# Kernel optimization log

Measured on AMD Instinct MI355X. Metric: run time of the kernel, lower is better.

## Reference

```python
import jax, jax.numpy as jnp
import numpy as np

B, N, D, H = 1, 512, 128, 128  # batch, n_res, d_pair, d_hid
EPS = 1e-5


def _layer_norm(x, w, b):
    m = jnp.mean(x, axis=-1, keepdims=True)
    v = jnp.mean(jnp.square(x - m), axis=-1, keepdims=True)
    return (x - m) * jax.lax.rsqrt(v + EPS) * w + b


def setup_inputs() -> dict:
    key = jax.random.key(0)
    ks = jax.random.split(key, 8)
    s = 0.02
    return {
        "z": jax.random.normal(ks[0], (B, N, N, D), dtype=jnp.float32),
        "mask": jnp.ones((B, N, N), dtype=jnp.float32),
        "ln_in_w": jnp.ones((D,), dtype=jnp.float32),
        "ln_in_b": jnp.zeros((D,), dtype=jnp.float32),
        "w_ab_p": jax.random.normal(ks[1], (2 * H, D), dtype=jnp.float32) * s,
        "b_ab_p": jnp.zeros((2 * H,), dtype=jnp.float32),
        "w_ab_g": jax.random.normal(ks[2], (2 * H, D), dtype=jnp.float32) * s,
        "b_ab_g": jnp.zeros((2 * H,), dtype=jnp.float32),
        "w_g": jax.random.normal(ks[3], (D, D), dtype=jnp.float32) * s,
        "ln_out_w": jnp.ones((H,), dtype=jnp.float32),
        "ln_out_b": jnp.zeros((H,), dtype=jnp.float32),
        "w_z": jax.random.normal(ks[4], (D, H), dtype=jnp.float32) * s,
    }


def reference(z, mask, ln_in_w, ln_in_b, w_ab_p, b_ab_p, w_ab_g, b_ab_g, w_g, ln_out_w, ln_out_b, w_z):
    # mask: [B,N,N] -> [B,N,N,1], scaled by N**-0.5 (non-alphafold-original mode)
    m = mask[..., None] * (mask.shape[-1] ** -0.5)
    zl = _layer_norm(z, ln_in_w, ln_in_b)              # [B,N,N,D]
    g = jnp.einsum('bijd,ed->bije', zl, w_g)           # gate logits, no bias
    ab = (jnp.einsum('bijd,hd->bijh', zl, w_ab_p) + b_ab_p) \
         * m * jax.nn.sigmoid(jnp.einsum('bijd,hd->bijh', zl, w_ab_g) + b_ab_g)
    a, b = jnp.split(ab, 2, axis=-1)                   # each [B,N,N,H]
    # outgoing triangle update: x[b,i,j,h] = sum_k a[b,i,k,h] * b[b,j,k,h]
    x = jnp.einsum('bikh,bjkh->bijh', a, b)
    x = _layer_norm(x, ln_out_w, ln_out_b)
    x = jnp.einsum('bijh,dh->bijd', x, w_z)            # linear_z, no bias
    return x, g
```

## Files before the change

### kernel.cpp

```cpp
#include <hip/hip_runtime.h>
#include <hip/hip_bf16.h>

#define NRES 512
#define DDIM 128
#define HDIM 128
#define NPOS (NRES * NRES)
#define PLANE ((size_t)HDIM * NPOS)
#define EPSF 1e-5f
#define INV_SQRT_N 0.044194173824159216f

typedef __attribute__((ext_vector_type(4))) float  floatx4;
typedef __attribute__((ext_vector_type(8))) short  shortx8;

__device__ __forceinline__ short f2bf(float f) {
    union { float f; unsigned u; } v; v.f = f;
    unsigned r = v.u + 0x7fffu + ((v.u >> 16) & 1u);
    return (short)(r >> 16);
}
__device__ __forceinline__ float bf2f(short s) {
    union { unsigned u; float f; } v; v.u = ((unsigned)(unsigned short)s) << 16;
    return v.f;
}

__global__ __launch_bounds__(256)
void prep_kernel(const float* __restrict__ wabp, const float* __restrict__ wabg,
                 const float* __restrict__ wg, short* __restrict__ wpk)
{
    const int i = blockIdx.x * 256 + threadIdx.x;
    float v;
    if (i < 65536) {
        const int j = i & 7, lane = (i >> 3) & 63, ks = (i >> 9) & 3, ni = (i >> 11) & 3;
        const int phase = (i >> 13) & 1, c = (i >> 14) & 1, grp = (i >> 15) & 1;
        const int h = grp * 128 + c * 64 + ni * 16 + (lane & 15);
        const int k = ks * 32 + ((lane >> 4) & 3) * 8 + j;
        v = (phase ? wabg : wabp)[h * 128 + k];
    } else {
        const int ii = i - 65536;
        const int j = ii & 7, lane = (ii >> 3) & 63, ks = (ii >> 9) & 3, ni = (ii >> 11) & 3;
        const int c = (ii >> 13) & 1;
        const int h = c * 64 + ni * 16 + (lane & 15);
        const int k = ks * 32 + ((lane >> 4) & 3) * 8 + j;
        v = wg[h * 128 + k];
    }
    wpk[i] = f2bf(v);
}

__global__ __launch_bounds__(256)
void ln_kernel(const float* __restrict__ z, const float* __restrict__ lw,
               const float* __restrict__ lb, short* __restrict__ zl)
{
    const int tid = threadIdx.x;
    const int r = tid >> 1, hf = tid & 1;
    const size_t row = (size_t)blockIdx.x * 128 + r;
    const float* zp = z + row * DDIM + hf * 64;
    float4 v[16];
    float s = 0.f, sq = 0.f;
    #pragma unroll
    for (int c = 0; c < 16; ++c) {
        v[c] = ((const float4*)zp)[c];
        s  += v[c].x + v[c].y + v[c].z + v[c].w;
        sq += v[c].x*v[c].x + v[c].y*v[c].y + v[c].z*v[c].z + v[c].w*v[c].w;
    }
    s  += __shfl_xor(s, 1);
    sq += __shfl_xor(sq, 1);
    const float mean = s * (1.f/128.f);
    const float var  = sq * (1.f/128.f) - mean * mean;
    const float inv  = rsqrtf(var + EPSF);
    short* op = zl + row * DDIM + hf * 64;
    #pragma unroll
    for (int c = 0; c < 16; ++c) {
        const int d = hf*64 + c*4;
        short4 o;
        o.x = f2bf((v[c].x - mean)*inv*lw[d+0] + lb[d+0]);
        o.y = f2bf((v[c].y - mean)*inv*lw[d+1] + lb[d+1]);
        o.z = f2bf((v[c].z - mean)*inv*lw[d+2] + lb[d+2]);
        o.w = f2bf((v[c].w - mean)*inv*lw[d+3] + lb[d+3]);
        *(short4*)(op + c*4) = o;
    }
}

__global__ __launch_bounds__(256)
void proj_kernel(const short* __restrict__ zl, const float* __restrict__ mask,
                 const short* __restrict__ wpk,
                 const float* __restrict__ b_ab_p, const float* __restrict__ b_ab_g,
                 float* __restrict__ g_out,
                 short* __restrict__ a_t, short* __restrict__ b_t)
{
    __shared__ short stage[64][136];
    const int tid = threadIdx.x, lane = tid & 63, wave = tid >> 6;
    const int lrow = lane & 15, quad = lane >> 4;
    const int chunk = blockIdx.x;
    const int pos0  = blockIdx.y * 128;

    shortx8 af[2][4];
    #pragma unroll
    for (int mi = 0; mi < 2; ++mi) {
        const short* ap = zl + (size_t)(pos0 + wave*32 + mi*16 + lrow) * DDIM + quad*8;
        #pragma unroll
        for (int ks = 0; ks < 4; ++ks)
            af[mi][ks] = *(const shortx8*)(ap + ks*32);
    }

    if (chunk < 4) {
        const int grp = chunk >> 1, c = chunk & 1;
        const short* pb = wpk + (size_t)((grp*2 + c)*2    ) * 8192 + lane*8;
        const short* gb = wpk + (size_t)((grp*2 + c)*2 + 1) * 8192 + lane*8;
        floatx4 accp[2][4], accg[2][4];
        #pragma unroll
        for (int mi = 0; mi < 2; ++mi)
            #pragma unroll
            for (int ni = 0; ni < 4; ++ni) {
                accp[mi][ni] = (floatx4){0.f,0.f,0.f,0.f};
                accg[mi][ni] = (floatx4){0.f,0.f,0.f,0.f};
            }
        #pragma unroll
        for (int ks = 0; ks < 4; ++ks)
            #pragma unroll
            for (int ni = 0; ni < 4; ++ni) {
                shortx8 bp = *(const shortx8*)(pb + (ni*4 + ks)*512);
                accp[0][ni] = __builtin_amdgcn_mfma_f32_16x16x32_bf16(af[0][ks], bp, accp[0][ni], 0,0,0);
                accp[1][ni] = __builtin_amdgcn_mfma_f32_16x16x32_bf16(af[1][ks], bp, accp[1][ni], 0,0,0);
                shortx8 bg = *(const shortx8*)(gb + (ni*4 + ks)*512);
                accg[0][ni] = __builtin_amdgcn_mfma_f32_16x16x32_bf16(af[0][ks], bg, accg[0][ni], 0,0,0);
                accg[1][ni] = __builtin_amdgcn_mfma_f32_16x16x32_bf16(af[1][ks], bg, accg[1][ni], 0,0,0);
            }
        const int hb0 = grp*128 + c*64;
        #pragma unroll
        for (int mi = 0; mi < 2; ++mi) {
            float mv[4];
            #pragma unroll
            for (int r = 0; r < 4; ++r)
                mv[r] = mask[pos0 + wave*32 + mi*16 + quad*4 + r] * INV_SQRT_N;
            #pragma unroll
            for (int ni = 0; ni < 4; ++ni) {
                const int col = ni*16 + lrow;
                const float bp = b_ab_p[hb0 + col];
                const float bg = b_ab_g[hb0 + col];
                #pragma unroll
                for (int r = 0; r < 4; ++r) {
                    const int row = wave*32 + mi*16 + quad*4 + r;
                    const float sig = 1.f / (1.f + __expf(-(accg[mi][ni][r] + bg)));
                    stage[col][row] = f2bf((accp[mi][ni][r] + bp) * sig * mv[r]);
                }
            }
        }
        __syncthreads();
        short* dst = ((grp == 0) ? a_t : b_t)
                   + (size_t)(c*64 + (tid >> 2)) * NPOS + pos0 + (tid & 3) * 32;
        const short* sp = &stage[tid >> 2][(tid & 3) * 32];
        #pragma unroll
        for (int q = 0; q < 4; ++q)
            ((int4*)dst)[q] = ((const int4*)sp)[q];
    } else {
        const int c = chunk - 4;
        const short* gg = wpk + 65536 + (size_t)c * 8192 + lane*8;
        floatx4 acc[2][4];
        #pragma unroll
        for (int mi = 0; mi < 2; ++mi)
            #pragma unroll
            for (int ni = 0; ni < 4; ++ni)
                acc[mi][ni] = (floatx4){0.f,0.f,0.f,0.f};
        #pragma unroll
        for (int ks = 0; ks < 4; ++ks)
            #pragma unroll
            for (int ni = 0; ni < 4; ++ni) {
                shortx8 bw = *(const shortx8*)(gg + (ni*4 + ks)*512);
                acc[0][ni] = __builtin_amdgcn_mfma_f32_16x16x32_bf16(af[0][ks], bw, acc[0][ni], 0,0,0);
                acc[1][ni] = __builtin_amdgcn_mfma_f32_16x16x32_bf16(af[1][ks], bw, acc[1][ni], 0,0,0);
            }
        #pragma unroll
        for (int mi = 0; mi < 2; ++mi)
            #pragma unroll
            for (int ni = 0; ni < 4; ++ni)
                #pragma unroll
                for (int r = 0; r < 4; ++r) {
                    const int row = wave*32 + mi*16 + quad*4 + r;
                    g_out[(size_t)(pos0 + row) * DDIM + c*64 + ni*16 + lrow] = acc[mi][ni][r];
                }
    }
}

__global__ __launch_bounds__(256)
void tri_kernel(const short* __restrict__ a_t, const short* __restrict__ b_t,
                short* __restrict__ xr)
{
    __shared__ short As[128][72];
    __shared__ short Bs[128][72];

    const int tid  = threadIdx.x;
    const int lane = tid & 63;
    const int wave = tid >> 6;
    const int i0 = blockIdx.x * 128;
    const int j0 = blockIdx.y * 128;
    const int h  = blockIdx.z;
    const short* A = a_t + (size_t)h * NPOS;
    const short* B = b_t + (size_t)h * NPOS;

    floatx4 acc[2][8];
    #pragma unroll
    for (int mi = 0; mi < 2; ++mi)
        #pragma unroll
        for (int ni = 0; ni < 8; ++ni)
            acc[mi][ni] = (floatx4){0.f, 0.f, 0.f, 0.f};

    const int lr = tid >> 1;
    const int lh = tid & 1;
    const int lrow = lane & 15;
    const int quad = lane >> 4;

    for (int k0 = 0; k0 < NRES; k0 += 64) {
        const short* pa = A + (size_t)(i0 + lr) * NRES + k0 + lh * 32;
        const short* pb = B + (size_t)(j0 + lr) * NRES + k0 + lh * 32;
        #pragma unroll
        for (int c = 0; c < 4; ++c) {
            *(int4*)&As[lr][lh*32 + c*8] = ((const int4*)pa)[c];
            *(int4*)&Bs[lr][lh*32 + c*8] = ((const int4*)pb)[c];
        }
        __syncthreads();
        #pragma unroll
        for (int ks = 0; ks < 2; ++ks) {
            shortx8 af0 = *(const shortx8*)&As[wave*32      + lrow][ks*32 + quad*8];
            shortx8 af1 = *(const shortx8*)&As[wave*32 + 16 + lrow][ks*32 + quad*8];
            #pragma unroll
            for (int ni = 0; ni < 8; ++ni) {
                shortx8 bf = *(const shortx8*)&Bs[ni*16 + lrow][ks*32 + quad*8];
                acc[0][ni] = __builtin_amdgcn_mfma_f32_16x16x32_bf16(af0, bf, acc[0][ni], 0, 0, 0);
                acc[1][ni] = __builtin_amdgcn_mfma_f32_16x16x32_bf16(af1, bf, acc[1][ni], 0, 0, 0);
            }
        }
        __syncthreads();
    }

    short* xp = xr + (size_t)h * NPOS;
    #pragma unroll
    for (int mi = 0; mi < 2; ++mi)
        #pragma unroll
        for (int ni = 0; ni < 8; ++ni)
            #pragma unroll
            for (int r = 0; r < 4; ++r) {
                const int row = wave*32 + mi*16 + quad*4 + r;
                const int col = ni*16 + lrow;
                xp[(size_t)(i0 + row) * NRES + j0 + col] = f2bf(acc[mi][ni][r]);
            }
}

__global__ __launch_bounds__(256)
void out_kernel(const short* __restrict__ xr,
                const float* __restrict__ ln_w, const float* __restrict__ ln_b,
                const float* __restrict__ w_z, float* __restrict__ x_out)
{
    __shared__ float xt[128][130];
    __shared__ short xln[128][136];
    __shared__ short Bw[128][136];
    __shared__ float red_s[2][128];
    __shared__ float red_q[2][128];
    __shared__ float mean_l[128];
    __shared__ float inv_l[128];

    const int tid  = threadIdx.x;
    const int lane = tid & 63;
    const int wave = tid >> 6;
    const int pos0 = blockIdx.x * 128;

    {
        const int hr = tid >> 1;
        const int hf = tid & 1;
        const short* sp = xr + (size_t)hr * NPOS + pos0 + hf * 64;
        #pragma unroll
        for (int c = 0; c < 8; ++c) {
            shortx8 v = ((const shortx8*)sp)[c];
            #pragma unroll
            for (int j = 0; j < 8; ++j)
                xt[hr][hf*64 + c*8 + j] = bf2f(v[j]);
        }
        const float* wp = w_z + (size_t)hr * HDIM + hf * 64;
        #pragma unroll
        for (int c = 0; c < 16; ++c) {
            float4 v = ((const float4*)wp)[c];
            short4 o;
            o.x = f2bf(v.x); o.y = f2bf(v.y); o.z = f2bf(v.z); o.w = f2bf(v.w);
            *(short4*)&Bw[hr][hf*64 + c*4] = o;
        }
    }
    __syncthreads();

    {
        const int p  = tid & 127;
        const int hf = tid >> 7;
        float s = 0.f, sq = 0.f;
        for (int hh = hf*64; hh < hf*64 + 64; ++hh) {
            const float v = xt[hh][p];
            s += v; sq += v * v;
        }
        red_s[hf][p] = s;
        red_q[hf][p] = sq;
    }
    __syncthreads();
    if (tid < 128) {
        const float s  = red_s[0][tid] + red_s[1][tid];
        const float sq = red_q[0][tid] + red_q[1][tid];
        const float mean = s * (1.f/128.f);
        const float var  = sq * (1.f/128.f) - mean * mean;
        mean_l[tid] = mean;
        inv_l[tid]  = rsqrtf(var + EPSF);
    }
    __syncthreads();

    {
        const int p  = tid & 127;
        const int hf = tid >> 7;
        const float mean = mean_l[p];
        const float inv  = inv_l[p];
        for (int hh = hf*64; hh < hf*64 + 64; hh += 2) {
            short2 o;
            o.x = f2bf((xt[hh  ][p] - mean) * inv * ln_w[hh  ] + ln_b[hh  ]);
            o.y = f2bf((xt[hh+1][p] - mean) * inv * ln_w[hh+1] + ln_b[hh+1]);
            *(short2*)&xln[p][hh] = o;
        }
    }
    __syncthreads();

    floatx4 acc[2][8];
    #pragma unroll
    for (int mi = 0; mi < 2; ++mi)
        #pragma unroll
        for (int ni = 0; ni < 8; ++ni)
            acc[mi][ni] = (floatx4){0.f,0.f,0.f,0.f};

    const int lrow = lane & 15;
    const int quad = lane >> 4;
    #pragma unroll
    for (int ks = 0; ks < 4; ++ks) {
        shortx8 af0 = *(const shortx8*)&xln[wave*32      + lrow][ks*32 + quad*8];
        shortx8 af1 = *(const shortx8*)&xln[wave*32 + 16 + lrow][ks*32 + quad*8];
        #pragma unroll
        for (int ni = 0; ni < 8; ++ni) {
            shortx8 bf = *(const shortx8*)&Bw[ni*16 + lrow][ks*32 + quad*8];
            acc[0][ni] = __builtin_amdgcn_mfma_f32_16x16x32_bf16(af0, bf, acc[0][ni], 0,0,0);
            acc[1][ni] = __builtin_amdgcn_mfma_f32_16x16x32_bf16(af1, bf, acc[1][ni], 0,0,0);
        }
    }
    #pragma unroll
    for (int mi = 0; mi < 2; ++mi)
        #pragma unroll
        for (int ni = 0; ni < 8; ++ni)
            #pragma unroll
            for (int r = 0; r < 4; ++r) {
                const int row = wave*32 + mi*16 + quad*4 + r;
                const int col = ni*16 + lrow;
                x_out[(size_t)(pos0 + row) * DDIM + col] = acc[mi][ni][r];
            }
}

extern "C" void kernel_launch(void* const* d_in, const int* in_sizes, int n_in,
                              void* d_out, int out_size, void* d_ws, size_t ws_size,
                              hipStream_t stream)
{
    const float* z        = (const float*)d_in[0];
    const float* mask     = (const float*)d_in[1];
    const float* ln_in_w  = (const float*)d_in[2];
    const float* ln_in_b  = (const float*)d_in[3];
    const float* w_ab_p   = (const float*)d_in[4];
    const float* b_ab_p   = (const float*)d_in[5];
    const float* w_ab_g   = (const float*)d_in[6];
    const float* b_ab_g   = (const float*)d_in[7];
    const float* w_g      = (const float*)d_in[8];
    const float* ln_out_w = (const float*)d_in[9];
    const float* ln_out_b = (const float*)d_in[10];
    const float* w_z      = (const float*)d_in[11];

    float* x_out = (float*)d_out;
    float* g_out = x_out + (size_t)NPOS * DDIM;

    short* a_t = (short*)d_ws;
    short* b_t = a_t + PLANE;
    short* zl  = b_t + PLANE;
    short* xr  = zl;
    short* wpk = (short*)x_out;

    prep_kernel<<<320, 256, 0, stream>>>(w_ab_p, w_ab_g, w_g, wpk);
    ln_kernel<<<NPOS/128, 256, 0, stream>>>(z, ln_in_w, ln_in_b, zl);
    proj_kernel<<<dim3(6, NPOS/128), 256, 0, stream>>>(zl, mask, wpk,
                                                       b_ab_p, b_ab_g,
                                                       g_out, a_t, b_t);
    tri_kernel<<<dim3(4, 4, 128), 256, 0, stream>>>(a_t, b_t, xr);
    out_kernel<<<NPOS/128, 256, 0, stream>>>(xr, ln_out_w, ln_out_b, w_z, x_out);
}
```

Measured before the change: 738.2 us.

## Fuse input layernorm into projection kernel and loop over output chunks

```diff
diff --git a/kernel.cpp b/kernel.cpp
--- a/kernel.cpp
+++ b/kernel.cpp
@@ -46,65 +46,64 @@
 }
 
 __global__ __launch_bounds__(256)
-void ln_kernel(const float* __restrict__ z, const float* __restrict__ lw,
-               const float* __restrict__ lb, short* __restrict__ zl)
-{
-    const int tid = threadIdx.x;
-    const int r = tid >> 1, hf = tid & 1;
-    const size_t row = (size_t)blockIdx.x * 128 + r;
-    const float* zp = z + row * DDIM + hf * 64;
-    float4 v[16];
-    float s = 0.f, sq = 0.f;
-    #pragma unroll
-    for (int c = 0; c < 16; ++c) {
-        v[c] = ((const float4*)zp)[c];
-        s  += v[c].x + v[c].y + v[c].z + v[c].w;
-        sq += v[c].x*v[c].x + v[c].y*v[c].y + v[c].z*v[c].z + v[c].w*v[c].w;
-    }
-    s  += __shfl_xor(s, 1);
-    sq += __shfl_xor(sq, 1);
-    const float mean = s * (1.f/128.f);
-    const float var  = sq * (1.f/128.f) - mean * mean;
-    const float inv  = rsqrtf(var + EPSF);
-    short* op = zl + row * DDIM + hf * 64;
-    #pragma unroll
-    for (int c = 0; c < 16; ++c) {
-        const int d = hf*64 + c*4;
-        short4 o;
-        o.x = f2bf((v[c].x - mean)*inv*lw[d+0] + lb[d+0]);
-        o.y = f2bf((v[c].y - mean)*inv*lw[d+1] + lb[d+1]);
-        o.z = f2bf((v[c].z - mean)*inv*lw[d+2] + lb[d+2]);
-        o.w = f2bf((v[c].w - mean)*inv*lw[d+3] + lb[d+3]);
-        *(short4*)(op + c*4) = o;
-    }
-}
-
-__global__ __launch_bounds__(256)
-void proj_kernel(const short* __restrict__ zl, const float* __restrict__ mask,
-                 const short* __restrict__ wpk,
-                 const float* __restrict__ b_ab_p, const float* __restrict__ b_ab_g,
-                 float* __restrict__ g_out,
-                 short* __restrict__ a_t, short* __restrict__ b_t)
+void lnproj_kernel(const float* __restrict__ z,
+                   const float* __restrict__ lw, const float* __restrict__ lb,
+                   const float* __restrict__ mask,
+                   const short* __restrict__ wpk,
+                   const float* __restrict__ b_ab_p, const float* __restrict__ b_ab_g,
+                   float* __restrict__ g_out,
+                   short* __restrict__ a_t, short* __restrict__ b_t)
 {
     __shared__ short stage[64][136];
     const int tid = threadIdx.x, lane = tid & 63, wave = tid >> 6;
     const int lrow = lane & 15, quad = lane >> 4;
-    const int chunk = blockIdx.x;
-    const int pos0  = blockIdx.y * 128;
+    const int pos0 = blockIdx.x * 128;
 
     shortx8 af[2][4];
     #pragma unroll
     for (int mi = 0; mi < 2; ++mi) {
-        const short* ap = zl + (size_t)(pos0 + wave*32 + mi*16 + lrow) * DDIM + quad*8;
-        #pragma unroll
-        for (int ks = 0; ks < 4; ++ks)
-            af[mi][ks] = *(const shortx8*)(ap + ks*32);
-    }
-
-    if (chunk < 4) {
+        const int row = pos0 + wave*32 + mi*16 + lrow;
+        const float* zp = z + (size_t)row * DDIM + quad*8;
+        float v[4][8];
+        float s = 0.f, sq = 0.f;
+        #pragma unroll
+        for (int ks = 0; ks < 4; ++ks) {
+            const float4 v0 = *(const float4*)(zp + ks*32);
+            const float4 v1 = *(const float4*)(zp + ks*32 + 4);
+            v[ks][0]=v0.x; v[ks][1]=v0.y; v[ks][2]=v0.z; v[ks][3]=v0.w;
+            v[ks][4]=v1.x; v[ks][5]=v1.y; v[ks][6]=v1.z; v[ks][7]=v1.w;
+            s  += v0.x+v0.y+v0.z+v0.w + v1.x+v1.y+v1.z+v1.w;
+            sq += v0.x*v0.x+v0.y*v0.y+v0.z*v0.z+v0.w*v0.w
+                + v1.x*v1.x+v1.y*v1.y+v1.z*v1.z+v1.w*v1.w;
+        }
+        s  += __shfl_xor(s, 16);  sq += __shfl_xor(sq, 16);
+        s  += __shfl_xor(s, 32);  sq += __shfl_xor(sq, 32);
+        const float mean = s * (1.f/128.f);
+        const float var  = sq * (1.f/128.f) - mean * mean;
+        const float inv  = rsqrtf(var + EPSF);
+        #pragma unroll
+        for (int ks = 0; ks < 4; ++ks) {
+            const int cb = ks*32 + quad*8;
+            shortx8 o;
+            #pragma unroll
+            for (int j = 0; j < 8; ++j)
+                o[j] = f2bf((v[ks][j] - mean) * inv * lw[cb+j] + lb[cb+j]);
+            af[mi][ks] = o;
+        }
+    }
+
+    float mv[2][4];
+    #pragma unroll
+    for (int mi = 0; mi < 2; ++mi)
+        #pragma unroll
+        for (int r = 0; r < 4; ++r)
+            mv[mi][r] = mask[pos0 + wave*32 + mi*16 + quad*4 + r] * INV_SQRT_N;
+
+    #pragma unroll 1
+    for (int chunk = 0; chunk < 4; ++chunk) {
         const int grp = chunk >> 1, c = chunk & 1;
-        const short* pb = wpk + (size_t)((grp*2 + c)*2    ) * 8192 + lane*8;
-        const short* gb = wpk + (size_t)((grp*2 + c)*2 + 1) * 8192 + lane*8;
+        const short* pb = wpk + (size_t)(chunk*2    ) * 8192 + lane*8;
+        const short* gb = wpk + (size_t)(chunk*2 + 1) * 8192 + lane*8;
         floatx4 accp[2][4], accg[2][4];
         #pragma unroll
         for (int mi = 0; mi < 2; ++mi)
@@ -125,12 +124,9 @@
                 accg[1][ni] = __builtin_amdgcn_mfma_f32_16x16x32_bf16(af[1][ks], bg, accg[1][ni], 0,0,0);
             }
         const int hb0 = grp*128 + c*64;
-        #pragma unroll
-        for (int mi = 0; mi < 2; ++mi) {
-            float mv[4];
-            #pragma unroll
-            for (int r = 0; r < 4; ++r)
-                mv[r] = mask[pos0 + wave*32 + mi*16 + quad*4 + r] * INV_SQRT_N;
+        __syncthreads();
+        #pragma unroll
+        for (int mi = 0; mi < 2; ++mi)
             #pragma unroll
             for (int ni = 0; ni < 4; ++ni) {
                 const int col = ni*16 + lrow;
@@ -140,10 +136,9 @@
                 for (int r = 0; r < 4; ++r) {
                     const int row = wave*32 + mi*16 + quad*4 + r;
                     const float sig = 1.f / (1.f + __expf(-(accg[mi][ni][r] + bg)));
-                    stage[col][row] = f2bf((accp[mi][ni][r] + bp) * sig * mv[r]);
+                    stage[col][row] = f2bf((accp[mi][ni][r] + bp) * sig * mv[mi][r]);
                 }
             }
-        }
         __syncthreads();
         short* dst = ((grp == 0) ? a_t : b_t)
                    + (size_t)(c*64 + (tid >> 2)) * NPOS + pos0 + (tid & 3) * 32;
@@ -151,8 +146,10 @@
         #pragma unroll
         for (int q = 0; q < 4; ++q)
             ((int4*)dst)[q] = ((const int4*)sp)[q];
-    } else {
-        const int c = chunk - 4;
+    }
+
+    #pragma unroll 1
+    for (int c = 0; c < 2; ++c) {
         const short* gg = wpk + 65536 + (size_t)c * 8192 + lane*8;
         floatx4 acc[2][4];
         #pragma unroll
@@ -374,15 +371,13 @@
 
     short* a_t = (short*)d_ws;
     short* b_t = a_t + PLANE;
-    short* zl  = b_t + PLANE;
-    short* xr  = zl;
+    short* xr  = b_t + PLANE;
     short* wpk = (short*)x_out;
 
     prep_kernel<<<320, 256, 0, stream>>>(w_ab_p, w_ab_g, w_g, wpk);
-    ln_kernel<<<NPOS/128, 256, 0, stream>>>(z, ln_in_w, ln_in_b, zl);
-    proj_kernel<<<dim3(6, NPOS/128), 256, 0, stream>>>(zl, mask, wpk,
-                                                       b_ab_p, b_ab_g,
-                                                       g_out, a_t, b_t);
+    lnproj_kernel<<<NPOS/128, 256, 0, stream>>>(z, ln_in_w, ln_in_b, mask, wpk,
+                                                b_ab_p, b_ab_g,
+                                                g_out, a_t, b_t);
     tri_kernel<<<dim3(4, 4, 128), 256, 0, stream>>>(a_t, b_t, xr);
     out_kernel<<<NPOS/128, 256, 0, stream>>>(xr, ln_out_w, ln_out_b, w_z, x_out);
 }
```

Measured after the change: 733.9 us. Within noise of the previous version (-0.6%).
